# Kernel tuning notes

Hardware: AMD Instinct MI355X
Metric: run time of the kernel (lower is better)

The kernel has to match this reference:

```python
import jax, jax.numpy as jnp
import numpy as np


def conv3d(x, w, b):
    # x: [B,C,T,H,W], w: [O,I,3,3,3], padding=1, stride=1
    y = jax.lax.conv_general_dilated(
        x, w, window_strides=(1, 1, 1), padding=((1, 1), (1, 1), (1, 1)),
        dimension_numbers=('NCDHW', 'OIDHW', 'NCDHW'))
    return y + b[None, :, None, None, None]


def deform_conv3d(x, offsets, w, b):
    # Deformable 3D conv, kernel 3, pad 1, stride 1, no modulation mask.
    # offsets: [B, 81, T, H, W] -> [B, 27, 3(t,h,w), T, H, W]
    B, Cin, T, H, W = x.shape
    nk = 27
    off = offsets.reshape(B, nk, 3, T, H, W)
    r = jnp.arange(3, dtype=x.dtype) - 1.0  # kernel taps {-1,0,1}
    kt, kh, kw = jnp.meshgrid(r, r, r, indexing='ij')
    koff = jnp.stack([kt.ravel(), kh.ravel(), kw.ravel()], axis=-1)  # [27,3]
    bt = jnp.arange(T, dtype=x.dtype)[:, None, None]
    bh = jnp.arange(H, dtype=x.dtype)[None, :, None]
    bw = jnp.arange(W, dtype=x.dtype)[None, None, :]
    base = jnp.stack(jnp.broadcast_arrays(bt, bh, bw), axis=0)  # [3,T,H,W]
    pos = base[None, None] + koff[None, :, :, None, None, None] + off  # [B,27,3,T,H,W]
    pt, ph, pw = pos[:, :, 0], pos[:, :, 1], pos[:, :, 2]
    ft, fh, fw = jnp.floor(pt), jnp.floor(ph), jnp.floor(pw)
    at, ah, aw = pt - ft, ph - fh, pw - fw
    it, ih, iw = ft.astype(jnp.int32), fh.astype(jnp.int32), fw.astype(jnp.int32)
    N = T * H * W
    xf = x.reshape(B, Cin, N)
    gather = jax.vmap(lambda xb, lb: xb[:, lb])  # ([Cin,N],[27,N])->[Cin,27,N]
    acc = jnp.zeros((B, Cin, nk, N), dtype=x.dtype)
    # trilinear interpolation: accumulate 8 corners, zero outside bounds
    for dt in (0, 1):
        tti = it + dt
        wt = (1.0 - at) if dt == 0 else at
        vt = (tti >= 0) & (tti < T)
        tc = jnp.clip(tti, 0, T - 1)
        for dh in (0, 1):
            hhi = ih + dh
            wh = (1.0 - ah) if dh == 0 else ah
            vh = (hhi >= 0) & (hhi < H)
            hc = jnp.clip(hhi, 0, H - 1)
            for dw in (0, 1):
                wwi = iw + dw
                ww = (1.0 - aw) if dw == 0 else aw
                vw = (wwi >= 0) & (wwi < W)
                wc = jnp.clip(wwi, 0, W - 1)
                wgt = (wt * wh * ww) * (vt & vh & vw).astype(x.dtype)  # [B,27,T,H,W]
                lin = (tc * H + hc) * W + wc  # [B,27,T,H,W]
                g = gather(xf, lin.reshape(B, nk, N))  # [B,Cin,27,N]
                acc = acc + wgt.reshape(B, 1, nk, N) * g
    out = jnp.einsum('oik,bikn->bon', w.reshape(w.shape[0], Cin, nk), acc)
    out = out + b[None, :, None]
    return out.reshape(B, w.shape[0], T, H, W)


def setup_inputs() -> dict:
    key = jax.random.key(0)
    ks = jax.random.split(key, 12)
    B, Cin, Cout, mdim = 1, 256, 256, 256
    T, H, W = 8, 24, 24

    def winit(k, shape):
        fan_in = int(np.prod(shape[1:]))
        return jax.random.normal(k, shape, jnp.float32) / np.float32(np.sqrt(fan_in))

    return {
        'x': jax.random.normal(ks[0], (B, Cin, T, H, W), jnp.float32),
        'l1_w': winit(ks[1], (mdim, Cin, 3, 3, 3)),
        'l1_b': jnp.zeros((mdim,), jnp.float32),
        'l2_w': winit(ks[2], (mdim, mdim, 3, 3, 3)),
        'l2_b': jnp.zeros((mdim,), jnp.float32),
        'l3_w': winit(ks[3], (mdim, mdim, 3, 3, 3)),
        'l3_b': jnp.zeros((mdim,), jnp.float32),
        'def_w': winit(ks[4], (81, mdim, 3, 3, 3)) * 0.1,  # keep offsets small
        'def_b': jnp.zeros((81,), jnp.float32),
        'c3d_w': winit(ks[5], (Cout, Cin, 3, 3, 3)),
        'c3d_b': jnp.zeros((Cout,), jnp.float32),
    }


def reference(x, l1_w, l1_b, l2_w, l2_b, l3_w, l3_b, def_w, def_b, c3d_w, c3d_b):
    h = jax.nn.relu(conv3d(x, l1_w, l1_b))
    h = jax.nn.relu(conv3d(h, l2_w, l2_b))
    h = jax.nn.relu(conv3d(h, l3_w, l3_b))
    offsets = conv3d(h, def_w, def_b)  # [B,81,T,H,W]
    return deform_conv3d(x, offsets, c3d_w, c3d_b)
```

## Files before the change

### kernel.cpp

```cpp
#include <hip/hip_runtime.h>

#define TT 8
#define HH 24
#define WW 24
#define NN 4608
#define CIN 256
#define N3 6760
#define KDIM 6912
#define BK 64
#define KTILES 108
#define NSPLIT 6
#define KT_PER 18

typedef short short8 __attribute__((ext_vector_type(8)));
typedef short short4v __attribute__((ext_vector_type(4)));
typedef float f32x4  __attribute__((ext_vector_type(4)));
typedef int   i32x4  __attribute__((ext_vector_type(4)));
typedef unsigned int u32x4 __attribute__((ext_vector_type(4)));

#define MFMA16 __builtin_amdgcn_mfma_f32_16x16x32_bf16

__device__ __forceinline__ short f2bf(float f) {
    unsigned u = __float_as_uint(f);
    unsigned r = u + 0x7fffu + ((u >> 16) & 1u);
    return (short)(r >> 16);
}

__device__ __forceinline__ int n3_of(int n) {
    int t = n / (HH * WW), r = n % (HH * WW), h = r / WW, w = r % WW;
    return ((t + 1) * 26 + (h + 1)) * 26 + (w + 1);
}

__device__ __forceinline__ void gload16(const void* gsrc, void* lds) {
    __builtin_amdgcn_global_load_lds(
        (const __attribute__((address_space(1))) void*)gsrc,
        (__attribute__((address_space(3))) void*)lds, 16, 0, 0);
}

__global__ __launch_bounds__(256) void transpose_k(const float* __restrict__ x,
                                                   short* __restrict__ xbf3) {
    __shared__ float T[64][65];
    const int lane = threadIdx.x & 63, wave = threadIdx.x >> 6;
    const int n0 = blockIdx.x * 64, ci0 = blockIdx.y * 64;
    #pragma unroll
    for (int j = 0; j < 16; ++j) {
        int ci_l = wave * 16 + j;
        T[ci_l][lane] = x[(size_t)(ci0 + ci_l) * NN + n0 + lane];
    }
    __syncthreads();
    #pragma unroll
    for (int j = 0; j < 16; ++j) {
        int n_l = wave * 16 + j;
        xbf3[(size_t)n3_of(n0 + n_l) * 256 + ci0 + lane] = f2bf(T[lane][n_l]);
    }
}

__global__ void repack_w_k(const float* __restrict__ w, short* __restrict__ dst, int Cout) {
    int o = blockIdx.x, ci = threadIdx.x;
    const int row = o & 127, y = o >> 7;
    #pragma unroll
    for (int k = 0; k < 27; ++k) {
        int K = k * 256 + ci;
        int kt = K >> 6, kk = K & 63;
        int slot = (kk >> 3) ^ (row & 7), e = kk & 7;
        size_t idx = ((size_t)(y * KTILES + kt)) * 8192 + row * 64 + slot * 8 + e;
        float v = (o < Cout) ? w[((size_t)o * CIN + ci) * 27 + k] : 0.f;
        dst[idx] = f2bf(v);
    }
}

__global__ __launch_bounds__(256) void sample_k(
    const short* __restrict__ xbf3, const float* __restrict__ offs,
    short* __restrict__ S)
{
    __shared__ char recs[64 * 64];
    const int k = blockIdx.y, n0 = blockIdx.x * 64;
    const int tid = threadIdx.x;

    if (tid < 64) {
        const int n = n0 + tid;
        const int t = n / (HH * WW), r = n % (HH * WW), h = r / WW, w2 = r % WW;
        const int ki = k / 9, kj = (k % 9) / 3, kl = k % 3;
        const float pt = (float)(t  + ki - 1) + offs[(size_t)(k * 3 + 0) * NN + n];
        const float ph = (float)(h  + kj - 1) + offs[(size_t)(k * 3 + 1) * NN + n];
        const float pw = (float)(w2 + kl - 1) + offs[(size_t)(k * 3 + 2) * NN + n];
        const float ft = floorf(pt), fh = floorf(ph), fw = floorf(pw);
        const float at = pt - ft, ah = ph - fh, aw = pw - fw;
        const int it = (int)ft, ih = (int)fh, iw = (int)fw;
        i32x4 idx[2]; f32x4 wgt[2];
        #pragma unroll
        for (int dt = 0; dt < 2; ++dt)
        #pragma unroll
        for (int dh = 0; dh < 2; ++dh)
        #pragma unroll
        for (int dw = 0; dw < 2; ++dw) {
            const int c = (dt * 2 + dh) * 2 + dw;
            const int ti = it + dt, hi = ih + dh, wi = iw + dw;
            const bool v = (ti >= 0) && (ti < TT) && (hi >= 0) && (hi < HH) && (wi >= 0) && (wi < WW);
            float wv = (dt ? at : 1.f - at) * (dh ? ah : 1.f - ah) * (dw ? aw : 1.f - aw);
            const int tc = min(max(ti, 0), TT - 1), hc = min(max(hi, 0), HH - 1), wc = min(max(wi, 0), WW - 1);
            const int r3 = ((tc + 1) * 26 + (hc + 1)) * 26 + (wc + 1);
            idx[c >> 2][c & 3] = r3 * 512;
            wgt[c >> 2][c & 3] = v ? wv : 0.f;
        }
        char* rec = &recs[tid * 64];
        *(i32x4*)(rec)      = idx[0];
        *(i32x4*)(rec + 16) = idx[1];
        *(f32x4*)(rec + 32) = wgt[0];
        *(f32x4*)(rec + 48) = wgt[1];
    }
    __syncthreads();

    const int lane = tid & 63, wave = tid >> 6;
    const int half = lane >> 5, lch = lane & 31;
    const char* xb = (const char*)xbf3 + lch * 16;
    short* Sk = S + (size_t)k * NN * 256 + lch * 8;

    for (int i = 0; i < 16; i += 4) {
        const int na = wave * 16 + i + half;
        const int nb = na + 2;
        const char* ra = &recs[na * 64];
        const char* rb = &recs[nb * 64];
        const i32x4 ia0 = *(const i32x4*)(ra);
        const i32x4 ia1 = *(const i32x4*)(ra + 16);
        const f32x4 wa0 = *(const f32x4*)(ra + 32);
        const f32x4 wa1 = *(const f32x4*)(ra + 48);
        const i32x4 ib0 = *(const i32x4*)(rb);
        const i32x4 ib1 = *(const i32x4*)(rb + 16);
        const f32x4 wb0 = *(const f32x4*)(rb + 32);
        const f32x4 wb1 = *(const f32x4*)(rb + 48);

        u32x4 ga[8], gb[8];
        #pragma unroll
        for (int c = 0; c < 4; ++c) {
            ga[c]     = *(const u32x4*)(xb + ia0[c]);
            ga[c + 4] = *(const u32x4*)(xb + ia1[c]);
            gb[c]     = *(const u32x4*)(xb + ib0[c]);
            gb[c + 4] = *(const u32x4*)(xb + ib1[c]);
        }

        float sa[8] = {}, sb[8] = {};
        #pragma unroll
        for (int c = 0; c < 8; ++c) {
            const float va = (c < 4) ? wa0[c & 3] : wa1[c & 3];
            const float vb = (c < 4) ? wb0[c & 3] : wb1[c & 3];
            #pragma unroll
            for (int j = 0; j < 4; ++j) {
                sa[2*j]   = fmaf(va, __uint_as_float(ga[c][j] << 16),         sa[2*j]);
                sa[2*j+1] = fmaf(va, __uint_as_float(ga[c][j] & 0xffff0000u), sa[2*j+1]);
                sb[2*j]   = fmaf(vb, __uint_as_float(gb[c][j] << 16),         sb[2*j]);
                sb[2*j+1] = fmaf(vb, __uint_as_float(gb[c][j] & 0xffff0000u), sb[2*j+1]);
            }
        }
        short8 oa, ob;
        #pragma unroll
        for (int m = 0; m < 8; ++m) { oa[m] = f2bf(sa[m]); ob[m] = f2bf(sb[m]); }
        *(short8*)(Sk + (size_t)(n0 + na) * 256) = oa;
        *(short8*)(Sk + (size_t)(n0 + nb) * 256) = ob;
    }
}

template<int CP>
__global__ __launch_bounds__(256, 3) void gemm_conv_sk(
    const short* __restrict__ src,
    const short* __restrict__ wrb_sw,
    float* __restrict__ P)
{
    __shared__ short Ap[8192];
    __shared__ short Bw[8192];
    const int tid = threadIdx.x;
    const int l = tid & 63, w = tid >> 6;
    const int n0 = blockIdx.x * 128, co0 = blockIdx.y * 128, split = blockIdx.z;
    const int wr = w >> 1, wc = w & 1;
    const int lm = l & 15, lq = l >> 4;
    const int rswz = (lm & 7) << 3;
    const int kt0 = split * KT_PER;

    const int colA = 8 * ((l & 7) ^ ((l >> 3) & 7));
    int r3[4];
    #pragma unroll
    for (int j = 0; j < 4; ++j)
        r3[j] = n3_of(n0 + w * 32 + j * 8 + (l >> 3));
    const short* bbase = wrb_sw + ((size_t)blockIdx.y * KTILES) * 8192 + (w * 4) * 512 + l * 8;

    f32x4 acc[4][4] = {};

    for (int i = 0; i < KT_PER; ++i) {
        const int kt = kt0 + i;
        const int k = kt >> 2, ci0 = (kt & 3) * 64;
        const int dt = k / 9 - 1, dh = (k % 9) / 3 - 1, dw = k % 3 - 1;
        const int d3 = (dt * 26 + dh) * 26 + dw;
        #pragma unroll
        for (int j = 0; j < 4; ++j)
            gload16(src + (size_t)(r3[j] + d3) * 256 + ci0 + colA, &Ap[(w * 4 + j) * 512]);
        const short* b = bbase + (size_t)kt * 8192;
        #pragma unroll
        for (int j = 0; j < 4; ++j)
            gload16(b + j * 512, &Bw[(w * 4 + j) * 512]);
        __syncthreads();
        #pragma unroll
        for (int ks = 0; ks < 2; ++ks) {
            const int c = (ks * 32 + lq * 8) ^ rswz;
            short8 a[4], bf[4];
            #pragma unroll
            for (int m = 0; m < 4; ++m)
                a[m] = *(const short8*)&Ap[(wr * 64 + m * 16 + lm) * 64 + c];
            #pragma unroll
            for (int nb = 0; nb < 4; ++nb)
                bf[nb] = *(const short8*)&Bw[(wc * 64 + nb * 16 + lm) * 64 + c];
            #pragma unroll
            for (int m = 0; m < 4; ++m)
            #pragma unroll
            for (int nb = 0; nb < 4; ++nb)
                acc[m][nb] = MFMA16(a[m], bf[nb], acc[m][nb], 0, 0, 0);
        }
        __syncthreads();
    }
    #pragma unroll
    for (int m = 0; m < 4; ++m)
    #pragma unroll
    for (int nb = 0; nb < 4; ++nb) {
        int co = co0 + wc * 64 + nb * 16 + lm;
        int n = n0 + wr * 64 + m * 16 + lq * 4;
        *(f32x4*)(P + ((size_t)split * CP + co) * NN + n) = acc[m][nb];
    }
}

__global__ __launch_bounds__(256, 3) void gemm_deform_sk(
    const short* __restrict__ S,
    const short* __restrict__ wrb_sw,
    float* __restrict__ P)
{
    __shared__ short Ap[8192];
    __shared__ short Bw[8192];
    const int tid = threadIdx.x;
    const int l = tid & 63, w = tid >> 6;
    const int n0 = blockIdx.x * 128, co0 = blockIdx.y * 128, split = blockIdx.z;
    const int wr = w >> 1, wc = w & 1;
    const int lm = l & 15, lq = l >> 4;
    const int rswz = (lm & 7) << 3;
    const int kt0 = split * KT_PER;

    const int colA = 8 * ((l & 7) ^ ((l >> 3) & 7));
    int rA[4];
    #pragma unroll
    for (int j = 0; j < 4; ++j)
        rA[j] = n0 + w * 32 + j * 8 + (l >> 3);
    const short* bbase = wrb_sw + ((size_t)blockIdx.y * KTILES) * 8192 + (w * 4) * 512 + l * 8;

    f32x4 acc[4][4] = {};

    for (int i = 0; i < KT_PER; ++i) {
        const int kt = kt0 + i;
        const int k = kt >> 2, ci0 = (kt & 3) * 64;
        #pragma unroll
        for (int j = 0; j < 4; ++j)
            gload16(S + ((size_t)k * NN + rA[j]) * 256 + ci0 + colA, &Ap[(w * 4 + j) * 512]);
        const short* b = bbase + (size_t)kt * 8192;
        #pragma unroll
        for (int j = 0; j < 4; ++j)
            gload16(b + j * 512, &Bw[(w * 4 + j) * 512]);
        __syncthreads();
        #pragma unroll
        for (int ks = 0; ks < 2; ++ks) {
            const int c = (ks * 32 + lq * 8) ^ rswz;
            short8 a[4], bf[4];
            #pragma unroll
            for (int m = 0; m < 4; ++m)
                a[m] = *(const short8*)&Ap[(wr * 64 + m * 16 + lm) * 64 + c];
            #pragma unroll
            for (int nb = 0; nb < 4; ++nb)
                bf[nb] = *(const short8*)&Bw[(wc * 64 + nb * 16 + lm) * 64 + c];
            #pragma unroll
            for (int m = 0; m < 4; ++m)
            #pragma unroll
            for (int nb = 0; nb < 4; ++nb)
                acc[m][nb] = MFMA16(a[m], bf[nb], acc[m][nb], 0, 0, 0);
        }
        __syncthreads();
    }
    #pragma unroll
    for (int m = 0; m < 4; ++m)
    #pragma unroll
    for (int nb = 0; nb < 4; ++nb) {
        int co = co0 + wc * 64 + nb * 16 + lm;
        int n = n0 + wr * 64 + m * 16 + lq * 4;
        *(f32x4*)(P + ((size_t)split * 256 + co) * NN + n) = acc[m][nb];
    }
}

template<bool RELU>
__global__ __launch_bounds__(256) void reduce_k(
    const float* __restrict__ P, const float* __restrict__ bias,
    float* __restrict__ dst, int Cout, int CP)
{
    int id = blockIdx.x * 256 + threadIdx.x;
    int total = Cout * (NN / 4);
    if (id >= total) return;
    int co = id / (NN / 4), n4 = id - co * (NN / 4);
    const float* p0 = P + ((size_t)co) * NN + n4 * 4;
    f32x4 v = *(const f32x4*)p0;
    #pragma unroll
    for (int s = 1; s < NSPLIT; ++s) {
        f32x4 u = *(const f32x4*)(p0 + (size_t)s * CP * NN);
        #pragma unroll
        for (int q = 0; q < 4; ++q) v[q] += u[q];
    }
    float bv = bias[co];
    #pragma unroll
    for (int q = 0; q < 4; ++q) {
        float f = v[q] + bv;
        if (RELU) f = fmaxf(f, 0.f);
        v[q] = f;
    }
    *(f32x4*)(dst + (size_t)co * NN + n4 * 4) = v;
}

__global__ __launch_bounds__(256) void reduce_bf3(
    const float* __restrict__ P, const float* __restrict__ bias,
    short* __restrict__ dst)
{
    __shared__ float T[64][65];
    const int lane = threadIdx.x & 63, wave = threadIdx.x >> 6;
    const int n0 = blockIdx.x * 64, co0 = blockIdx.y * 64;
    #pragma unroll
    for (int j = 0; j < 16; ++j) {
        int co_l = wave * 16 + j, co = co0 + co_l;
        const float* p0 = P + (size_t)co * NN + n0 + lane;
        float a = p0[0];
        #pragma unroll
        for (int s = 1; s < NSPLIT; ++s) a += p0[(size_t)s * 256 * NN];
        T[co_l][lane] = fmaxf(a + bias[co], 0.f);
    }
    __syncthreads();
    #pragma unroll
    for (int j = 0; j < 16; ++j) {
        int n_l = wave * 16 + j;
        dst[(size_t)n3_of(n0 + n_l) * 256 + co0 + lane] = f2bf(T[lane][n_l]);
    }
}

extern "C" void kernel_launch(void* const* d_in, const int* in_sizes, int n_in,
                              void* d_out, int out_size, void* d_ws, size_t ws_size,
                              hipStream_t stream)
{
    const float* x   = (const float*)d_in[0];
    const float* l1w = (const float*)d_in[1];
    const float* l1b = (const float*)d_in[2];
    const float* l2w = (const float*)d_in[3];
    const float* l2b = (const float*)d_in[4];
    const float* l3w = (const float*)d_in[5];
    const float* l3b = (const float*)d_in[6];
    const float* dfw = (const float*)d_in[7];
    const float* dfb = (const float*)d_in[8];
    const float* c3w = (const float*)d_in[9];
    const float* c3b = (const float*)d_in[10];
    float* out = (float*)d_out;

    char* base = (char*)d_ws;
    short* S    = (short*)base;
    short* h1b  = (short*)(base);
    short* h2b  = (short*)(base + 3461120);
    short* h3b  = (short*)(base + 6922240);
    short* wrb1 = (short*)(base + 10383360);
    short* wrb2 = (short*)(base + 13922304);
    short* wrb3 = (short*)(base + 17461248);
    short* wrbd = (short*)(base + 21000192);
    char* q = base + 63700992;
    short* xbf3 = (short*)q; q += 3461120;
    float* offs = (float*)q; q += 1492992;
    short* wrbc = (short*)q; q += 3538944;
    float* P    = (float*)q;

    hipMemsetAsync(xbf3, 0, (size_t)N3 * 256 * 2, stream);
    hipMemsetAsync(h1b,  0, (size_t)3 * N3 * 256 * 2, stream);

    transpose_k<<<dim3(72, 4), dim3(256), 0, stream>>>(x, xbf3);
    repack_w_k<<<dim3(256), dim3(256), 0, stream>>>(l1w, wrb1, 256);
    repack_w_k<<<dim3(256), dim3(256), 0, stream>>>(l2w, wrb2, 256);
    repack_w_k<<<dim3(256), dim3(256), 0, stream>>>(l3w, wrb3, 256);
    repack_w_k<<<dim3(256), dim3(256), 0, stream>>>(c3w, wrbc, 256);
    repack_w_k<<<dim3(128), dim3(256), 0, stream>>>(dfw, wrbd, 81);

    const dim3 blk(256);
    const int rg81 = (81 * (NN / 4) + 255) / 256;
    const int rg256 = (256 * (NN / 4) + 255) / 256;

    gemm_conv_sk<256><<<dim3(36, 2, NSPLIT), blk, 0, stream>>>(xbf3, wrb1, P);
    reduce_bf3       <<<dim3(72, 4),         blk, 0, stream>>>(P, l1b, h1b);
    gemm_conv_sk<256><<<dim3(36, 2, NSPLIT), blk, 0, stream>>>(h1b, wrb2, P);
    reduce_bf3       <<<dim3(72, 4),         blk, 0, stream>>>(P, l2b, h2b);
    gemm_conv_sk<256><<<dim3(36, 2, NSPLIT), blk, 0, stream>>>(h2b, wrb3, P);
    reduce_bf3       <<<dim3(72, 4),         blk, 0, stream>>>(P, l3b, h3b);
    gemm_conv_sk<128><<<dim3(36, 1, NSPLIT), blk, 0, stream>>>(h3b, wrbd, P);
    reduce_k<false>  <<<dim3(rg81),          blk, 0, stream>>>(P, dfb, offs, 81, 128);

    sample_k<<<dim3(72, 27), blk, 0, stream>>>(xbf3, offs, S);
    gemm_deform_sk<<<dim3(36, 2, NSPLIT), blk, 0, stream>>>(S, wrbc, P);
    reduce_k<false><<<dim3(rg256), blk, 0, stream>>>(P, c3b, out, 256, 256);
}
```

Measured before the change: 231.4 us.

## Store split-K partials as bf16, raise split count, merge weight repacks

Split-K partial sums are now written as bf16 instead of fp32, which halves the traffic for partial writes and for the reduction reads. The split count goes from 6 to 9 to put more blocks on the GPU. The five weight-repack launches are merged into one kernel indexed by blockIdx.y to cut launch overhead. Rounding each partial to bf16 adds error to the accumulated result and may threaten tolerance.

```diff
diff --git a/kernel.cpp b/kernel.cpp
--- a/kernel.cpp
+++ b/kernel.cpp
@@ -9,8 +9,8 @@
 #define KDIM 6912
 #define BK 64
 #define KTILES 108
-#define NSPLIT 6
-#define KT_PER 18
+#define NSPLIT 9
+#define KT_PER 12
 
 typedef short short8 __attribute__((ext_vector_type(8)));
 typedef short short4v __attribute__((ext_vector_type(4)));
@@ -25,6 +25,9 @@
     unsigned r = u + 0x7fffu + ((u >> 16) & 1u);
     return (short)(r >> 16);
 }
+__device__ __forceinline__ float bf2f(short s) {
+    return __uint_as_float(((unsigned)(unsigned short)s) << 16);
+}
 
 __device__ __forceinline__ int n3_of(int n) {
     int t = n / (HH * WW), r = n % (HH * WW), h = r / WW, w = r % WW;
@@ -55,8 +58,19 @@
     }
 }
 
-__global__ void repack_w_k(const float* __restrict__ w, short* __restrict__ dst, int Cout) {
-    int o = blockIdx.x, ci = threadIdx.x;
+__global__ void repack_all_k(const float* __restrict__ w1, const float* __restrict__ w2,
+                             const float* __restrict__ w3, const float* __restrict__ wc,
+                             const float* __restrict__ wd,
+                             short* __restrict__ d1, short* __restrict__ d2,
+                             short* __restrict__ d3, short* __restrict__ dc,
+                             short* __restrict__ dd) {
+    const int sel = blockIdx.y, o = blockIdx.x, ci = threadIdx.x;
+    const float* w; short* dst; int Cout = 256;
+    if      (sel == 0) { w = w1; dst = d1; }
+    else if (sel == 1) { w = w2; dst = d2; }
+    else if (sel == 2) { w = w3; dst = d3; }
+    else if (sel == 3) { w = wc; dst = dc; }
+    else               { w = wd; dst = dd; Cout = 81; if (o >= 128) return; }
     const int row = o & 127, y = o >> 7;
     #pragma unroll
     for (int k = 0; k < 27; ++k) {
@@ -164,7 +178,7 @@
 __global__ __launch_bounds__(256, 3) void gemm_conv_sk(
     const short* __restrict__ src,
     const short* __restrict__ wrb_sw,
-    float* __restrict__ P)
+    short* __restrict__ P)
 {
     __shared__ short Ap[8192];
     __shared__ short Bw[8192];
@@ -222,14 +236,17 @@
     for (int nb = 0; nb < 4; ++nb) {
         int co = co0 + wc * 64 + nb * 16 + lm;
         int n = n0 + wr * 64 + m * 16 + lq * 4;
-        *(f32x4*)(P + ((size_t)split * CP + co) * NN + n) = acc[m][nb];
+        short4v o;
+        #pragma unroll
+        for (int j = 0; j < 4; ++j) o[j] = f2bf(acc[m][nb][j]);
+        *(short4v*)(P + ((size_t)split * CP + co) * NN + n) = o;
     }
 }
 
 __global__ __launch_bounds__(256, 3) void gemm_deform_sk(
     const short* __restrict__ S,
     const short* __restrict__ wrb_sw,
-    float* __restrict__ P)
+    short* __restrict__ P)
 {
     __shared__ short Ap[8192];
     __shared__ short Bw[8192];
@@ -285,39 +302,43 @@
     for (int nb = 0; nb < 4; ++nb) {
         int co = co0 + wc * 64 + nb * 16 + lm;
         int n = n0 + wr * 64 + m * 16 + lq * 4;
-        *(f32x4*)(P + ((size_t)split * 256 + co) * NN + n) = acc[m][nb];
+        short4v o;
+        #pragma unroll
+        for (int j = 0; j < 4; ++j) o[j] = f2bf(acc[m][nb][j]);
+        *(short4v*)(P + ((size_t)split * 256 + co) * NN + n) = o;
     }
 }
 
 template<bool RELU>
 __global__ __launch_bounds__(256) void reduce_k(
-    const float* __restrict__ P, const float* __restrict__ bias,
+    const short* __restrict__ P, const float* __restrict__ bias,
     float* __restrict__ dst, int Cout, int CP)
 {
     int id = blockIdx.x * 256 + threadIdx.x;
     int total = Cout * (NN / 4);
     if (id >= total) return;
     int co = id / (NN / 4), n4 = id - co * (NN / 4);
-    const float* p0 = P + ((size_t)co) * NN + n4 * 4;
-    f32x4 v = *(const f32x4*)p0;
-    #pragma unroll
-    for (int s = 1; s < NSPLIT; ++s) {
-        f32x4 u = *(const f32x4*)(p0 + (size_t)s * CP * NN);
-        #pragma unroll
-        for (int q = 0; q < 4; ++q) v[q] += u[q];
+    const short* p0 = P + ((size_t)co) * NN + n4 * 4;
+    float v[4] = {};
+    #pragma unroll
+    for (int s = 0; s < NSPLIT; ++s) {
+        short4v u = *(const short4v*)(p0 + (size_t)s * CP * NN);
+        #pragma unroll
+        for (int q = 0; q < 4; ++q) v[q] += bf2f(u[q]);
     }
     float bv = bias[co];
+    f32x4 o;
     #pragma unroll
     for (int q = 0; q < 4; ++q) {
         float f = v[q] + bv;
         if (RELU) f = fmaxf(f, 0.f);
-        v[q] = f;
-    }
-    *(f32x4*)(dst + (size_t)co * NN + n4 * 4) = v;
+        o[q] = f;
+    }
+    *(f32x4*)(dst + (size_t)co * NN + n4 * 4) = o;
 }
 
 __global__ __launch_bounds__(256) void reduce_bf3(
-    const float* __restrict__ P, const float* __restrict__ bias,
+    const short* __restrict__ P, const float* __restrict__ bias,
     short* __restrict__ dst)
 {
     __shared__ float T[64][65];
@@ -326,10 +347,10 @@
     #pragma unroll
     for (int j = 0; j < 16; ++j) {
         int co_l = wave * 16 + j, co = co0 + co_l;
-        const float* p0 = P + (size_t)co * NN + n0 + lane;
-        float a = p0[0];
-        #pragma unroll
-        for (int s = 1; s < NSPLIT; ++s) a += p0[(size_t)s * 256 * NN];
+        const short* p0 = P + (size_t)co * NN + n0 + lane;
+        float a = 0.f;
+        #pragma unroll
+        for (int s = 0; s < NSPLIT; ++s) a += bf2f(p0[(size_t)s * 256 * NN]);
         T[co_l][lane] = fmaxf(a + bias[co], 0.f);
     }
     __syncthreads();
@@ -370,17 +391,14 @@
     short* xbf3 = (short*)q; q += 3461120;
     float* offs = (float*)q; q += 1492992;
     short* wrbc = (short*)q; q += 3538944;
-    float* P    = (float*)q;
+    short* P    = (short*)q;
 
     hipMemsetAsync(xbf3, 0, (size_t)N3 * 256 * 2, stream);
     hipMemsetAsync(h1b,  0, (size_t)3 * N3 * 256 * 2, stream);
 
     transpose_k<<<dim3(72, 4), dim3(256), 0, stream>>>(x, xbf3);
-    repack_w_k<<<dim3(256), dim3(256), 0, stream>>>(l1w, wrb1, 256);
-    repack_w_k<<<dim3(256), dim3(256), 0, stream>>>(l2w, wrb2, 256);
-    repack_w_k<<<dim3(256), dim3(256), 0, stream>>>(l3w, wrb3, 256);
-    repack_w_k<<<dim3(256), dim3(256), 0, stream>>>(c3w, wrbc, 256);
-    repack_w_k<<<dim3(128), dim3(256), 0, stream>>>(dfw, wrbd, 81);
+    repack_all_k<<<dim3(256, 5), dim3(256), 0, stream>>>(l1w, l2w, l3w, c3w, dfw,
+                                                         wrb1, wrb2, wrb3, wrbc, wrbd);
 
     const dim3 blk(256);
     const int rg81 = (81 * (NN / 4) + 255) / 256;
```

Result: no change. 232.2 us (+0.3%).
